# Kernel tuning notes

Measured on AMD Instinct MI355X. Metric: run time of the kernel, lower is better.

Reference implementation:

```python
import jax, jax.numpy as jnp
import numpy as np

N, DIM, K = 65536, 512, 256


def setup_inputs() -> dict:
    key = jax.random.key(0)
    k1, k2 = jax.random.split(key)
    embeddings = jax.random.normal(k1, (N, DIM), dtype=jnp.float32)
    # Centroid table produced by the (external, non-differentiable) faiss
    # k-means fit; materialized here as a learned parameter.
    centroids = jax.random.normal(k2, (K, DIM), dtype=jnp.float32)
    return {"embeddings": embeddings, "centroids": centroids, "batch_id": 0}


def reference(embeddings, centroids, batch_id):
    # Batched equivalent of the Python loop over samples:
    # for each embedding, cdist to centroids, take the 2nd-nearest centroid.
    # Squared L2 preserves the ordering of torch.cdist (monotone sqrt),
    # and the output is a gather of centroids, so math is identical.
    # d2: [N, K]
    d2 = (
        jnp.sum(embeddings * embeddings, axis=1, keepdims=True)
        - 2.0 * jnp.einsum("nd,kd->nk", embeddings, centroids)
        + jnp.sum(centroids * centroids, axis=1)
    )
    # top-2 smallest distances -> indices of nearest and 2nd-nearest centroids
    _, top2_idx = jax.lax.top_k(-d2, 2)  # [N, 2]
    hard_neg_idx = top2_idx[:, 1]  # second-nearest centroid per sample
    return centroids[hard_neg_idx]  # [N, DIM]
```

## Files before the change

### kernel.cpp

```cpp
#include <hip/hip_runtime.h>

#define N_EMB 65536
#define DIM   512
#define K_C   256


typedef __attribute__((ext_vector_type(4))) float        f32x4;
typedef __attribute__((ext_vector_type(8))) __bf16       bf16x8;
typedef __attribute__((ext_vector_type(8))) short        s16x8;
typedef __attribute__((ext_vector_type(4))) unsigned int u32x4;

template <class T>
__device__ inline auto mfma_bf16_t(T a, T b, f32x4 c, int)
    -> decltype(__builtin_amdgcn_mfma_f32_16x16x32_bf16(a, b, c, 0, 0, 0)) {
  return __builtin_amdgcn_mfma_f32_16x16x32_bf16(a, b, c, 0, 0, 0);
}
template <class T>
__device__ inline f32x4 mfma_bf16_t(T a, T b, f32x4 c, long) {
  return __builtin_amdgcn_mfma_f32_16x16x32_bf16(
      __builtin_bit_cast(s16x8, a), __builtin_bit_cast(s16x8, b), c, 0, 0, 0);
}
__device__ inline f32x4 MFMA(bf16x8 a, bf16x8 b, f32x4 c) {
  return mfma_bf16_t(a, b, c, 0);
}

__device__ inline unsigned umin_(unsigned a, unsigned b) { return a < b ? a : b; }
__device__ inline unsigned umax_(unsigned a, unsigned b) { return a > b ? a : b; }

__device__ inline void cvt8(const float4 a, const float4 b, u32x4& hw, u32x4& lw) {
  float v[8] = {a.x, a.y, a.z, a.w, b.x, b.y, b.z, b.w};
  unsigned h[8], l[8];
#pragma unroll
  for (int i = 0; i < 8; ++i) {
    const unsigned u  = __float_as_uint(v[i]);
    const unsigned hb = (u + 0x7FFFu + ((u >> 16) & 1u)) >> 16;
    h[i] = hb;
    const float hf = __uint_as_float(hb << 16);
    const unsigned ul = __float_as_uint(v[i] - hf);
    l[i] = (ul + 0x7FFFu + ((ul >> 16) & 1u)) >> 16;
  }
  hw = (u32x4){h[0] | (h[1] << 16), h[2] | (h[3] << 16),
               h[4] | (h[5] << 16), h[6] | (h[7] << 16)};
  lw = (u32x4){l[0] | (l[1] << 16), l[2] | (l[3] << 16),
               l[4] | (l[5] << 16), l[6] | (l[7] << 16)};
}

__global__ void pack_centroids(const float* __restrict__ cent, unsigned* __restrict__ cbg) {
  const int k    = blockIdx.x;
  const int lane = threadIdx.x;
  const float* src = cent + (size_t)k * DIM + lane * 8;
  u32x4 hw, lw;
  cvt8(*(const float4*)src, *(const float4*)(src + 4), hw, lw);
  const int chunk = lane >> 2;
  const int fl    = (lane & 3) * 16 + (k & 15);
  const int ct    = k >> 4;
  u32x4* base = (u32x4*)cbg;
  base[(((size_t)chunk * 2 + 0) * 16 + ct) * 64 + fl] = hw;
  base[(((size_t)chunk * 2 + 1) * 16 + ct) * 64 + fl] = lw;
}

__global__ void centroid_norms(const float* __restrict__ cent,
                               float* __restrict__ cnorm) {
  const int k = blockIdx.x;
  const int lane = threadIdx.x;
  const float4* row = (const float4*)(cent + (size_t)k * DIM);
  float s = 0.f;
  for (int i = lane; i < DIM / 4; i += 64) {
    float4 v = row[i];
    s += v.x * v.x + v.y * v.y + v.z * v.z + v.w * v.w;
  }
#pragma unroll
  for (int off = 32; off > 0; off >>= 1) s += __shfl_down(s, off, 64);
  if (lane == 0) cnorm[k] = s;
}

__global__ __launch_bounds__(512, 2)
void neg_sampler_main(const float* __restrict__ emb,
                      const float* __restrict__ cent,
                      const unsigned* __restrict__ cbg,
                      const float* __restrict__ cnorm,
                      float* __restrict__ out) {
  extern __shared__ char lds[];
  char* const EH = lds;
  char* const EL = lds + 16384;
  char* const CB = lds + 32768;

  const int tid  = threadIdx.x;
  const int lane = tid & 63;
  const int w    = tid >> 6;
  const int row0 = blockIdx.x * 256;

  f32x4 acc[2][16];
#pragma unroll
  for (int i = 0; i < 2; ++i)
#pragma unroll
    for (int j = 0; j < 16; ++j) acc[i][j] = (f32x4){0.f, 0.f, 0.f, 0.f};

  const int er  = tid & 255;
  const int eg0 = tid >> 8;
  const float* const ebase = emb + (size_t)(row0 + er) * DIM;
  const int et = er >> 4, erow = er & 15;
  const int eoffA = et * 1024 + (eg0 * 16 + erow) * 16;
  const int eoffB = et * 1024 + ((eg0 + 2) * 16 + erow) * 16;

  float4 ev0, ev1, ev2, ev3;
  u32x4  cv0, cv1, cv2, cv3;

  auto load_chunk = [&](int c) {
    const float* p0 = ebase + c * 32 + eg0 * 8;
    ev0 = *(const float4*)p0;
    ev1 = *(const float4*)(p0 + 4);
    ev2 = *(const float4*)(p0 + 16);
    ev3 = *(const float4*)(p0 + 20);
    const u32x4* cs = (const u32x4*)cbg + (size_t)c * 2048 + tid;
    cv0 = cs[0]; cv1 = cs[512]; cv2 = cs[1024]; cv3 = cs[1536];
  };
  auto store_chunk = [&]() {
    u32x4 hw, lw;
    cvt8(ev0, ev1, hw, lw);
    *(u32x4*)(EH + eoffA) = hw; *(u32x4*)(EL + eoffA) = lw;
    cvt8(ev2, ev3, hw, lw);
    *(u32x4*)(EH + eoffB) = hw; *(u32x4*)(EL + eoffB) = lw;
    u32x4* cd = (u32x4*)CB + tid;
    cd[0] = cv0; cd[512] = cv1; cd[1024] = cv2; cd[1536] = cv3;
  };

  load_chunk(0);
  for (int c = 0; c < 16; ++c) {
    if (c) __syncthreads();
    store_chunk();
    if (c < 15) load_chunk(c + 1);
    asm volatile("s_waitcnt lgkmcnt(0)" ::: "memory");
    __builtin_amdgcn_sched_barrier(0);
    __builtin_amdgcn_s_barrier();
    asm volatile("" ::: "memory");

    const char* ehp = EH + (2 * w) * 1024 + lane * 16;
    const char* elp = EL + (2 * w) * 1024 + lane * 16;
    const bf16x8 eh0 = *(const bf16x8*)ehp;
    const bf16x8 eh1 = *(const bf16x8*)(ehp + 1024);
    const bf16x8 el0 = *(const bf16x8*)elp;
    const bf16x8 el1 = *(const bf16x8*)(elp + 1024);
    const char* cbp = CB + lane * 16;
#pragma unroll
    for (int ct = 0; ct < 16; ++ct) {
      const bf16x8 ch = *(const bf16x8*)(cbp + ct * 1024);
      const bf16x8 cl = *(const bf16x8*)(cbp + 16384 + ct * 1024);
      acc[0][ct] = MFMA(eh0, ch, acc[0][ct]);
      acc[1][ct] = MFMA(eh1, ch, acc[1][ct]);
      acc[0][ct] = MFMA(el0, ch, acc[0][ct]);
      acc[1][ct] = MFMA(el1, ch, acc[1][ct]);
      acc[0][ct] = MFMA(eh0, cl, acc[0][ct]);
      acc[1][ct] = MFMA(eh1, cl, acc[1][ct]);
    }
  }
  __syncthreads();

  unsigned* top4 = (unsigned*)lds;
  const int lgrp = lane >> 4, lcol = lane & 15;
  float cnv[16];
#pragma unroll
  for (int ct = 0; ct < 16; ++ct) cnv[ct] = cnorm[ct * 16 + lcol];

#pragma unroll
  for (int rt = 0; rt < 2; ++rt) {
#pragma unroll
    for (int rg = 0; rg < 4; ++rg) {
      unsigned b0 = 0xFFFFFFFFu, b1 = b0, b2 = b0, b3 = b0;
      auto ins = [&](unsigned u) {
        b3 = umin_(b3, umax_(b2, u));
        b2 = umin_(b2, umax_(b1, u));
        b1 = umin_(b1, umax_(b0, u));
        b0 = umin_(b0, u);
      };
#pragma unroll
      for (int ct = 0; ct < 16; ++ct) {
        const float s = fmaf(-2.f, acc[rt][ct][rg], cnv[ct]);
        ins((__float_as_uint(s) & 0xFFFFFF00u) | (unsigned)(ct * 16 + lcol));
      }
#pragma unroll
      for (int off = 1; off < 16; off <<= 1) {
        const unsigned o0 = __shfl_xor(b0, off, 64);
        const unsigned o1 = __shfl_xor(b1, off, 64);
        const unsigned o2 = __shfl_xor(b2, off, 64);
        const unsigned o3 = __shfl_xor(b3, off, 64);
        ins(o0); ins(o1); ins(o2); ins(o3);
      }
      if (lcol == 0) {
        const int row = w * 32 + rt * 16 + lgrp * 4 + rg;
        *(u32x4*)(top4 + row * 4) = (u32x4){b0, b1, b2, b3};
      }
    }
  }
  __syncthreads();

  for (int rr = 0; rr < 32; ++rr) {
    const int row  = w * 32 + rr;
    const int grow = row0 + row;
    const float* ep = emb + (size_t)grow * DIM + lane * 8;
    const float4 e0 = *(const float4*)ep;
    const float4 e1 = *(const float4*)(ep + 4);
    int cand[4];
    float sc[4];
#pragma unroll
    for (int j = 0; j < 4; ++j) cand[j] = (int)(top4[row * 4 + j] & 0xFFu);
#pragma unroll
    for (int j = 0; j < 4; ++j) {
      const float* cp = cent + (size_t)cand[j] * DIM + lane * 8;
      const float4 c0 = *(const float4*)cp;
      const float4 c1 = *(const float4*)(cp + 4);
      float d = e0.x * c0.x;
      d = fmaf(e0.y, c0.y, d); d = fmaf(e0.z, c0.z, d); d = fmaf(e0.w, c0.w, d);
      d = fmaf(e1.x, c1.x, d); d = fmaf(e1.y, c1.y, d);
      d = fmaf(e1.z, c1.z, d); d = fmaf(e1.w, c1.w, d);
#pragma unroll
      for (int off = 1; off < 64; off <<= 1) d += __shfl_xor(d, off, 64);
      sc[j] = fmaf(-2.f, d, cnorm[cand[j]]);
    }
    float v1 = 3.4e38f, v2 = 3.4e38f;
    int i1 = K_C, i2 = K_C;
#pragma unroll
    for (int j = 0; j < 4; ++j) {
      const float s = sc[j];
      const int ci = cand[j];
      if (s < v1 || (s == v1 && ci < i1)) { v2 = v1; i2 = i1; v1 = s; i1 = ci; }
      else if (s < v2 || (s == v2 && ci < i2)) { v2 = s; i2 = ci; }
    }
    const float* sp = cent + (size_t)i2 * DIM + lane * 8;
    const float4 o0 = *(const float4*)sp;
    const float4 o1 = *(const float4*)(sp + 4);
    float* op = out + (size_t)grow * DIM + lane * 8;
    *(float4*)op       = o0;
    *(float4*)(op + 4) = o1;
  }
}

extern "C" void kernel_launch(void* const* d_in, const int* in_sizes, int n_in,
                              void* d_out, int out_size, void* d_ws, size_t ws_size,
                              hipStream_t stream) {
  const float* emb  = (const float*)d_in[0];
  const float* cent = (const float*)d_in[1];
  unsigned* cbg = (unsigned*)d_ws;
  float* cnorm  = (float*)((char*)d_ws + 512 * 1024);

  pack_centroids<<<K_C, 64, 0, stream>>>(cent, cbg);
  centroid_norms<<<K_C, 64, 0, stream>>>(cent, cnorm);
  neg_sampler_main<<<N_EMB / 256, 512, 65536, stream>>>(emb, cent, cbg, cnorm,
                                                        (float*)d_out);
}
```

Before: 323.3 us.

## Drop centroid low-bf16 term, fuse norm kernel, halve block rows, lane-split rescoring

```diff
diff --git a/kernel.cpp b/kernel.cpp
--- a/kernel.cpp
+++ b/kernel.cpp
@@ -3,6 +3,8 @@
 #define N_EMB 65536
 #define DIM   512
 #define K_C   256
+#define ROWS  128
+#define NCHUNK (DIM / 32)
 
 
 typedef __attribute__((ext_vector_type(4))) float        f32x4;
@@ -45,50 +47,51 @@
                l[4] | (l[5] << 16), l[6] | (l[7] << 16)};
 }
 
-__global__ void pack_centroids(const float* __restrict__ cent, unsigned* __restrict__ cbg) {
+__device__ inline u32x4 cvt8hi(const float4 a, const float4 b) {
+  float v[8] = {a.x, a.y, a.z, a.w, b.x, b.y, b.z, b.w};
+  unsigned h[8];
+#pragma unroll
+  for (int i = 0; i < 8; ++i) {
+    const unsigned u = __float_as_uint(v[i]);
+    h[i] = (u + 0x7FFFu + ((u >> 16) & 1u)) >> 16;
+  }
+  return (u32x4){h[0] | (h[1] << 16), h[2] | (h[3] << 16),
+                 h[4] | (h[5] << 16), h[6] | (h[7] << 16)};
+}
+
+__global__ void pack_centroids(const float* __restrict__ cent,
+                               unsigned* __restrict__ cbh,
+                               float* __restrict__ cnorm) {
   const int k    = blockIdx.x;
   const int lane = threadIdx.x;
   const float* src = cent + (size_t)k * DIM + lane * 8;
-  u32x4 hw, lw;
-  cvt8(*(const float4*)src, *(const float4*)(src + 4), hw, lw);
-  const int chunk = lane >> 2;
-  const int fl    = (lane & 3) * 16 + (k & 15);
-  const int ct    = k >> 4;
-  u32x4* base = (u32x4*)cbg;
-  base[(((size_t)chunk * 2 + 0) * 16 + ct) * 64 + fl] = hw;
-  base[(((size_t)chunk * 2 + 1) * 16 + ct) * 64 + fl] = lw;
-}
-
-__global__ void centroid_norms(const float* __restrict__ cent,
-                               float* __restrict__ cnorm) {
-  const int k = blockIdx.x;
-  const int lane = threadIdx.x;
-  const float4* row = (const float4*)(cent + (size_t)k * DIM);
-  float s = 0.f;
-  for (int i = lane; i < DIM / 4; i += 64) {
-    float4 v = row[i];
-    s += v.x * v.x + v.y * v.y + v.z * v.z + v.w * v.w;
-  }
+  const float4 a = *(const float4*)src;
+  const float4 b = *(const float4*)(src + 4);
+  const int chunk = lane >> 2, g = lane & 3;
+  ((u32x4*)cbh)[((size_t)chunk * 16 + (k >> 4)) * 64 + g * 16 + (k & 15)] =
+      cvt8hi(a, b);
+  float s = a.x * a.x + a.y * a.y + a.z * a.z + a.w * a.w +
+            b.x * b.x + b.y * b.y + b.z * b.z + b.w * b.w;
 #pragma unroll
   for (int off = 32; off > 0; off >>= 1) s += __shfl_down(s, off, 64);
   if (lane == 0) cnorm[k] = s;
 }
 
-__global__ __launch_bounds__(512, 2)
+__global__ __launch_bounds__(256, 2)
 void neg_sampler_main(const float* __restrict__ emb,
                       const float* __restrict__ cent,
-                      const unsigned* __restrict__ cbg,
+                      const unsigned* __restrict__ cbh,
                       const float* __restrict__ cnorm,
                       float* __restrict__ out) {
   extern __shared__ char lds[];
   char* const EH = lds;
-  char* const EL = lds + 16384;
-  char* const CB = lds + 32768;
+  char* const EL = lds + 8192;
+  char* const CB = lds + 16384;
 
   const int tid  = threadIdx.x;
   const int lane = tid & 63;
   const int w    = tid >> 6;
-  const int row0 = blockIdx.x * 256;
+  const int row0 = blockIdx.x * ROWS;
 
   f32x4 acc[2][16];
 #pragma unroll
@@ -96,24 +99,24 @@
 #pragma unroll
     for (int j = 0; j < 16; ++j) acc[i][j] = (f32x4){0.f, 0.f, 0.f, 0.f};
 
-  const int er  = tid & 255;
-  const int eg0 = tid >> 8;
+  const int er = tid & 127;
+  const int g0 = (tid >> 7) * 2;
   const float* const ebase = emb + (size_t)(row0 + er) * DIM;
   const int et = er >> 4, erow = er & 15;
-  const int eoffA = et * 1024 + (eg0 * 16 + erow) * 16;
-  const int eoffB = et * 1024 + ((eg0 + 2) * 16 + erow) * 16;
+  const int eoffA = et * 1024 + (g0 * 16 + erow) * 16;
+  const int eoffB = et * 1024 + ((g0 + 1) * 16 + erow) * 16;
 
   float4 ev0, ev1, ev2, ev3;
   u32x4  cv0, cv1, cv2, cv3;
 
   auto load_chunk = [&](int c) {
-    const float* p0 = ebase + c * 32 + eg0 * 8;
+    const float* p0 = ebase + c * 32 + g0 * 8;
     ev0 = *(const float4*)p0;
     ev1 = *(const float4*)(p0 + 4);
-    ev2 = *(const float4*)(p0 + 16);
-    ev3 = *(const float4*)(p0 + 20);
-    const u32x4* cs = (const u32x4*)cbg + (size_t)c * 2048 + tid;
-    cv0 = cs[0]; cv1 = cs[512]; cv2 = cs[1024]; cv3 = cs[1536];
+    ev2 = *(const float4*)(p0 + 8);
+    ev3 = *(const float4*)(p0 + 12);
+    const u32x4* cs = (const u32x4*)cbh + (size_t)c * 1024 + tid;
+    cv0 = cs[0]; cv1 = cs[256]; cv2 = cs[512]; cv3 = cs[768];
   };
   auto store_chunk = [&]() {
     u32x4 hw, lw;
@@ -122,14 +125,14 @@
     cvt8(ev2, ev3, hw, lw);
     *(u32x4*)(EH + eoffB) = hw; *(u32x4*)(EL + eoffB) = lw;
     u32x4* cd = (u32x4*)CB + tid;
-    cd[0] = cv0; cd[512] = cv1; cd[1024] = cv2; cd[1536] = cv3;
+    cd[0] = cv0; cd[256] = cv1; cd[512] = cv2; cd[768] = cv3;
   };
 
   load_chunk(0);
-  for (int c = 0; c < 16; ++c) {
+  for (int c = 0; c < NCHUNK; ++c) {
     if (c) __syncthreads();
     store_chunk();
-    if (c < 15) load_chunk(c + 1);
+    if (c < NCHUNK - 1) load_chunk(c + 1);
     asm volatile("s_waitcnt lgkmcnt(0)" ::: "memory");
     __builtin_amdgcn_sched_barrier(0);
     __builtin_amdgcn_s_barrier();
@@ -145,13 +148,10 @@
 #pragma unroll
     for (int ct = 0; ct < 16; ++ct) {
       const bf16x8 ch = *(const bf16x8*)(cbp + ct * 1024);
-      const bf16x8 cl = *(const bf16x8*)(cbp + 16384 + ct * 1024);
       acc[0][ct] = MFMA(eh0, ch, acc[0][ct]);
       acc[1][ct] = MFMA(eh1, ch, acc[1][ct]);
       acc[0][ct] = MFMA(el0, ch, acc[0][ct]);
       acc[1][ct] = MFMA(el1, ch, acc[1][ct]);
-      acc[0][ct] = MFMA(eh0, cl, acc[0][ct]);
-      acc[1][ct] = MFMA(eh1, cl, acc[1][ct]);
     }
   }
   __syncthreads();
@@ -197,41 +197,43 @@
   for (int rr = 0; rr < 32; ++rr) {
     const int row  = w * 32 + rr;
     const int grow = row0 + row;
-    const float* ep = emb + (size_t)grow * DIM + lane * 8;
-    const float4 e0 = *(const float4*)ep;
-    const float4 e1 = *(const float4*)(ep + 4);
-    int cand[4];
-    float sc[4];
-#pragma unroll
-    for (int j = 0; j < 4; ++j) cand[j] = (int)(top4[row * 4 + j] & 0xFFu);
-#pragma unroll
-    for (int j = 0; j < 4; ++j) {
-      const float* cp = cent + (size_t)cand[j] * DIM + lane * 8;
-      const float4 c0 = *(const float4*)cp;
-      const float4 c1 = *(const float4*)(cp + 4);
-      float d = e0.x * c0.x;
-      d = fmaf(e0.y, c0.y, d); d = fmaf(e0.z, c0.z, d); d = fmaf(e0.w, c0.w, d);
-      d = fmaf(e1.x, c1.x, d); d = fmaf(e1.y, c1.y, d);
-      d = fmaf(e1.z, c1.z, d); d = fmaf(e1.w, c1.w, d);
-#pragma unroll
-      for (int off = 1; off < 64; off <<= 1) d += __shfl_xor(d, off, 64);
-      sc[j] = fmaf(-2.f, d, cnorm[cand[j]]);
+    const unsigned t0 = top4[row * 4 + 0], t1 = top4[row * 4 + 1];
+    const unsigned t2 = top4[row * 4 + 2], t3 = top4[row * 4 + 3];
+    const int c0 = (int)(t0 & 0xFFu), c1 = (int)(t1 & 0xFFu);
+    const int c2 = (int)(t2 & 0xFFu), c3 = (int)(t3 & 0xFFu);
+    const int cj = lane >> 4, li = lane & 15;
+    const int myc = cj == 0 ? c0 : cj == 1 ? c1 : cj == 2 ? c2 : c3;
+
+    const float4* e4 = (const float4*)(emb + (size_t)grow * DIM);
+    const float4* c4 = (const float4*)(cent + (size_t)myc * DIM);
+    float d = 0.f;
+#pragma unroll
+    for (int i = 0; i < 8; ++i) {
+      const float4 ev = e4[li + 16 * i];
+      const float4 cv = c4[li + 16 * i];
+      d = fmaf(ev.x, cv.x, d); d = fmaf(ev.y, cv.y, d);
+      d = fmaf(ev.z, cv.z, d); d = fmaf(ev.w, cv.w, d);
     }
-    float v1 = 3.4e38f, v2 = 3.4e38f;
-    int i1 = K_C, i2 = K_C;
-#pragma unroll
-    for (int j = 0; j < 4; ++j) {
-      const float s = sc[j];
-      const int ci = cand[j];
-      if (s < v1 || (s == v1 && ci < i1)) { v2 = v1; i2 = i1; v1 = s; i1 = ci; }
-      else if (s < v2 || (s == v2 && ci < i2)) { v2 = s; i2 = ci; }
-    }
-    const float* sp = cent + (size_t)i2 * DIM + lane * 8;
-    const float4 o0 = *(const float4*)sp;
-    const float4 o1 = *(const float4*)(sp + 4);
-    float* op = out + (size_t)grow * DIM + lane * 8;
-    *(float4*)op       = o0;
-    *(float4*)(op + 4) = o1;
+#pragma unroll
+    for (int off = 1; off < 16; off <<= 1) d += __shfl_xor(d, off, 64);
+
+    const float s0 = fmaf(-2.f, __shfl(d, 0, 64),  cnorm[c0]);
+    const float s1 = fmaf(-2.f, __shfl(d, 16, 64), cnorm[c1]);
+    const float s2 = fmaf(-2.f, __shfl(d, 32, 64), cnorm[c2]);
+    const float s3 = fmaf(-2.f, __shfl(d, 48, 64), cnorm[c3]);
+
+    float v1 = s0, v2 = 3.4e38f;
+    int i1 = c0, i2 = K_C;
+    auto upd = [&](float s, int c) {
+      if (s < v1 || (s == v1 && c < i1)) { v2 = v1; i2 = i1; v1 = s; i1 = c; }
+      else if (s < v2 || (s == v2 && c < i2)) { v2 = s; i2 = c; }
+    };
+    upd(s1, c1); upd(s2, c2); upd(s3, c3);
+
+    const float4* sp = (const float4*)(cent + (size_t)i2 * DIM) + lane * 2;
+    float4* op = (float4*)(out + (size_t)grow * DIM) + lane * 2;
+    op[0] = sp[0];
+    op[1] = sp[1];
   }
 }
 
@@ -240,11 +242,10 @@
                               hipStream_t stream) {
   const float* emb  = (const float*)d_in[0];
   const float* cent = (const float*)d_in[1];
-  unsigned* cbg = (unsigned*)d_ws;
-  float* cnorm  = (float*)((char*)d_ws + 512 * 1024);
-
-  pack_centroids<<<K_C, 64, 0, stream>>>(cent, cbg);
-  centroid_norms<<<K_C, 64, 0, stream>>>(cent, cnorm);
-  neg_sampler_main<<<N_EMB / 256, 512, 65536, stream>>>(emb, cent, cbg, cnorm,
-                                                        (float*)d_out);
-}
+  unsigned* cbh = (unsigned*)d_ws;
+  float* cnorm  = (float*)((char*)d_ws + 256 * 1024);
+
+  pack_centroids<<<K_C, 64, 0, stream>>>(cent, cbh, cnorm);
+  neg_sampler_main<<<N_EMB / ROWS, 256, 32768, stream>>>(emb, cent, cbh, cnorm,
+                                                         (float*)d_out);
+}
```

Measured after the change: 327.8 us. No clear change (+1.4%).
